# Kernel optimization log

Measured on AMD Instinct MI355X. Metric: run time of the kernel, lower is better.

Reference implementation:

```python
import jax, jax.numpy as jnp
import numpy as np


def bilinear_align_corners(p, H, W):
    # p: [B, C, h, w] -> [B, C, H, W], matches F.interpolate(mode='bilinear', align_corners=True)
    b, c, h, w = p.shape
    ys = jnp.linspace(0.0, h - 1.0, H)
    xs = jnp.linspace(0.0, w - 1.0, W)
    y0 = jnp.floor(ys).astype(jnp.int32)
    x0 = jnp.floor(xs).astype(jnp.int32)
    y1 = jnp.minimum(y0 + 1, h - 1)
    x1 = jnp.minimum(x0 + 1, w - 1)
    wy = (ys - y0.astype(p.dtype))[:, None]          # [H,1]
    wx = (xs - x0.astype(p.dtype))                   # [W]
    rows = p[:, :, y0, :] * (1 - wy) + p[:, :, y1, :] * wy   # [B,C,H,w]
    out = rows[:, :, :, x0] * (1 - wx) + rows[:, :, :, x1] * wx  # [B,C,H,W]
    return out


def conv1x1(x, W, b):
    return jnp.einsum('bchw,oc->bohw', x, W) + b[None, :, None, None]


def scan_axis(feat, A_bar, B_bar, axis):
    # selective recurrence h_i = A_i * stop_grad(h_{i-1}) + B_i * x_i along `axis`
    f = jnp.moveaxis(feat, axis, 0)
    A = jnp.moveaxis(A_bar, axis, 0)
    B = jnp.moveaxis(B_bar, axis, 0)

    def step(prev, inp):
        a_i, b_i, x_i = inp
        h = a_i * jax.lax.stop_gradient(prev) + b_i * x_i
        return h, h

    _, hs = jax.lax.scan(step, jnp.zeros_like(f[0]), (A, B, f))
    return jnp.moveaxis(hs, 0, axis)


def setup_inputs() -> dict:
    key = jax.random.key(0)
    ks = jax.random.split(key, 12)
    Bsz, Cin, H, W = 4, 64, 256, 256
    hid = 128
    s_in = 1.0 / np.sqrt(Cin)
    s_hid = 1.0 / np.sqrt(hid)
    return {
        'x': jax.random.normal(ks[0], (Bsz, Cin, H, W), jnp.float32),
        'prior': jax.random.normal(ks[1], (Bsz, 1, 64, 64), jnp.float32),
        'W_in': jax.random.uniform(ks[2], (hid, Cin), jnp.float32, -s_in, s_in),
        'b_in': jax.random.uniform(ks[3], (hid,), jnp.float32, -s_in, s_in),
        'W_out': jax.random.uniform(ks[4], (Cin, hid), jnp.float32, -s_hid, s_hid),
        'b_out': jax.random.uniform(ks[5], (Cin,), jnp.float32, -s_hid, s_hid),
        'W_delta': jax.random.uniform(ks[6], (hid, hid), jnp.float32, -s_hid, s_hid),
        'b_delta': jax.random.uniform(ks[7], (hid,), jnp.float32, -s_hid, s_hid),
        'W_B': jax.random.uniform(ks[8], (hid, hid), jnp.float32, -s_hid, s_hid),
        'b_B': jax.random.uniform(ks[9], (hid,), jnp.float32, -s_hid, s_hid),
        'A_param': jax.random.normal(ks[10], (hid,), jnp.float32),
        'lambda_delta': jnp.float32(0.1),
        'alpha': jnp.float32(0.1),
        'gamma': jnp.float32(0.1),
    }


def reference(x, prior, W_in, b_in, W_out, b_out, W_delta, b_delta, W_B, b_B,
              A_param, lambda_delta, alpha, gamma):
    Bsz, C, H, W = x.shape
    prior_up = jnp.clip(bilinear_align_corners(prior, H, W), -1.0, 1.0)
    x_proj = conv1x1(x, W_in, b_in)
    delta = jax.nn.softplus(conv1x1(x_proj, W_delta, b_delta) + lambda_delta * prior_up)
    B_k = conv1x1(x_proj, W_B, b_B) * (1.0 + alpha * prior_up)
    A = -jnp.exp(A_param)[None, :, None, None]
    A_bar = jnp.exp(delta * A)
    B_bar = delta * B_k
    # dim=0 in torch code scans along W (axis 3); dim=1 scans along H (axis 2)
    scanned = scan_axis(x_proj, A_bar, B_bar, 3) + scan_axis(x_proj, A_bar, B_bar, 2)
    out = conv1x1(scanned, W_out, b_out)
    return (x + gamma * out, prior_up)
```

## Files before the change

kernel.cpp:

```cpp
#include <hip/hip_runtime.h>
#include <hip/hip_bf16.h>

#define OUT1 16777216
#define BIG  33554432

typedef _Float16 half8 __attribute__((ext_vector_type(8)));
typedef float    floatx4 __attribute__((ext_vector_type(4)));

struct __align__(8) h4s { _Float16 x, y, z, w; };
__device__ inline void store4h(_Float16* p, float4 v){
    h4s t; t.x = (_Float16)v.x; t.y = (_Float16)v.y; t.z = (_Float16)v.z; t.w = (_Float16)v.w;
    *(h4s*)p = t;
}

__global__ __launch_bounds__(256) void k_prior(const float* __restrict__ prior, float* __restrict__ pu){
    int i = blockIdx.x*256 + threadIdx.x;
    int b = i >> 16;
    int rem = i & 65535;
    int yy = rem >> 8, xx = rem & 255;
    const float scale = 63.0f/255.0f;
    float sy = yy*scale, sx = xx*scale;
    int y0 = min((int)floorf(sy), 63), x0 = min((int)floorf(sx), 63);
    int y1 = min(y0+1, 63), x1 = min(x0+1, 63);
    float wy = sy - (float)y0, wx = sx - (float)x0;
    const float* pb = prior + (b<<12);
    float v00 = pb[(y0<<6)+x0], v01 = pb[(y0<<6)+x1];
    float v10 = pb[(y1<<6)+x0], v11 = pb[(y1<<6)+x1];
    float r0 = v00*(1.f-wy) + v10*wy;
    float r1 = v01*(1.f-wy) + v11*wy;
    float v  = r0*(1.f-wx) + r1*wx;
    pu[i] = fminf(fmaxf(v, -1.f), 1.f);
}

__global__ __launch_bounds__(256) void k_comb(const float* __restrict__ W_in, const float* __restrict__ b_in,
        const float* __restrict__ W_delta, const float* __restrict__ b_delta,
        const float* __restrict__ W_B, const float* __restrict__ b_B,
        const float* __restrict__ A_param, const float* __restrict__ W_out,
        _Float16* __restrict__ Wch, float* __restrict__ bcv, float* __restrict__ negA,
        _Float16* __restrict__ Wof, float* __restrict__ bct){
    int i = blockIdx.x*256 + threadIdx.x;
    if (i < 24576){
        int r = i >> 6, c = i & 63;
        float v;
        if (r < 128) v = W_in[i];
        else if (r < 256){
            int rr = r-128; float s = 0.f;
            for (int k=0;k<128;k++) s = fmaf(W_delta[(rr<<7)+k], W_in[(k<<6)+c], s);
            v = s;
        } else {
            int rr = r-256; float s = 0.f;
            for (int k=0;k<128;k++) s = fmaf(W_B[(rr<<7)+k], W_in[(k<<6)+c], s);
            v = s;
        }
        Wch[i] = (_Float16)v;
    } else if (i < 24960){
        int r = i - 24576; float v;
        if (r < 128) v = b_in[r];
        else if (r < 256){
            int rr=r-128; float s = b_delta[rr];
            for (int k=0;k<128;k++) s = fmaf(W_delta[(rr<<7)+k], b_in[k], s);
            v = s;
        } else {
            int rr=r-256; float s = b_B[rr];
            for (int k=0;k<128;k++) s = fmaf(W_B[(rr<<7)+k], b_in[k], s);
            v = s;
        }
        bcv[r] = v;
    } else if (i < 25088){
        negA[i-24960] = -expf(A_param[i-24960]);
    } else if (i < 33280){
        Wof[i-25088] = (_Float16)W_out[i-25088];
    } else if (i < 33792){
        int j = i - 33280;
        int c = j >> 2, comp = j & 3;
        float v;
        if (comp == 0) v = b_in[c];
        else if (comp == 1){
            float s = b_delta[c];
            for (int k=0;k<128;k++) s = fmaf(W_delta[(c<<7)+k], b_in[k], s);
            v = s;
        } else if (comp == 2){
            float s = b_B[c];
            for (int k=0;k<128;k++) s = fmaf(W_B[(c<<7)+k], b_in[k], s);
            v = s;
        } else {
            v = -expf(A_param[c]);
        }
        bct[j] = v;
    }
}

__global__ __launch_bounds__(512, 4) void k_proj_mfma(const float* __restrict__ x, const float* __restrict__ pu,
        const _Float16* __restrict__ Wch, const float* __restrict__ bct,
        const float* __restrict__ lam_p, const float* __restrict__ alp_p,
        _Float16* __restrict__ Ab, _Float16* __restrict__ Uu){
    __shared__ _Float16 Ws[24576];

    const int t    = threadIdx.x;
    const int lane = t & 63;
    const int wave = t >> 6;
    const int col  = lane & 15;
    const int quad = lane >> 4;

    const int bl      = blockIdx.x;
    const int b       = bl >> 7;
    const int px_base = (bl & 127) << 9;

    {
        const float4* wsrc = (const float4*)Wch;
        #pragma unroll
        for (int i = 0; i < 6; i++){
            int c = t + (i << 9);
            int row = c >> 3, part = c & 7;
            float4 v = wsrc[c];
            int byteoff = ((row << 7) + (part << 4)) ^ ((row & 7) << 4);
            *(float4*)((char*)Ws + byteoff) = v;
        }
    }

    const float lamv = lam_p[0], alpv = alp_p[0];
    const float* xcol = x + ((size_t)b<<22) + col;

    float xf0[8], xf1[8];
    {
        const float* xp = xcol + px_base + (wave<<4);
        #pragma unroll
        for (int j = 0; j < 8; j++){
            xf0[j] = xp[(size_t)(quad*8 + j) << 16];
            xf1[j] = xp[(size_t)(quad*8 + j + 32) << 16];
        }
    }

    __syncthreads();

    const int qb = quad << 4;
    const char* wsb = (const char*)Ws;

    #pragma unroll 1
    for (int ch = 0; ch < 4; ch++){
        const int pxw = px_base + (ch << 7) + (wave << 4);

        half8 aX0, aX1;
        #pragma unroll
        for (int j = 0; j < 8; j++){
            aX0[j] = (_Float16)xf0[j];
            aX1[j] = (_Float16)xf1[j];
        }

        if (ch < 3){
            const float* xn = xcol + pxw + 128;
            #pragma unroll
            for (int j = 0; j < 8; j++){
                xf0[j] = xn[(size_t)(quad*8 + j) << 16];
                xf1[j] = xn[(size_t)(quad*8 + j + 32) << 16];
            }
        }

        float4 puv4 = *(const float4*)(pu + (b<<16) + pxw + (quad<<2));
        float lpu[4], apu[4];
        #pragma unroll
        for (int r = 0; r < 4; r++){
            float pv = ((const float*)&puv4)[r];
            lpu[r] = lamv * pv;
            apu[r] = fmaf(alpv, pv, 1.f);
        }

        #pragma unroll 2
        for (int ct = 0; ct < 8; ct++){
            int rI = (ct << 4) + col;
            int xr = (rI & 7) << 4;
            half8 wI0 = *(const half8*)(wsb + ((( rI       << 7) +      qb) ^ xr));
            half8 wI1 = *(const half8*)(wsb + ((( rI       << 7) + 64 + qb) ^ xr));
            half8 wD0 = *(const half8*)(wsb + ((((rI + 128)<< 7) +      qb) ^ xr));
            half8 wD1 = *(const half8*)(wsb + ((((rI + 128)<< 7) + 64 + qb) ^ xr));
            half8 wB0 = *(const half8*)(wsb + ((((rI + 256)<< 7) +      qb) ^ xr));
            half8 wB1 = *(const half8*)(wsb + ((((rI + 256)<< 7) + 64 + qb) ^ xr));

            floatx4 aI = (floatx4){0.f,0.f,0.f,0.f};
            floatx4 aD = (floatx4){0.f,0.f,0.f,0.f};
            floatx4 aB = (floatx4){0.f,0.f,0.f,0.f};
            aI = __builtin_amdgcn_mfma_f32_16x16x32_f16(aX0, wI0, aI, 0, 0, 0);
            aD = __builtin_amdgcn_mfma_f32_16x16x32_f16(aX0, wD0, aD, 0, 0, 0);
            aB = __builtin_amdgcn_mfma_f32_16x16x32_f16(aX0, wB0, aB, 0, 0, 0);
            aI = __builtin_amdgcn_mfma_f32_16x16x32_f16(aX1, wI1, aI, 0, 0, 0);
            aD = __builtin_amdgcn_mfma_f32_16x16x32_f16(aX1, wD1, aD, 0, 0, 0);
            aB = __builtin_amdgcn_mfma_f32_16x16x32_f16(aX1, wB1, aB, 0, 0, 0);

            int c = (ct<<4) + col;
            float4 bv = *(const float4*)(bct + (c<<2));
            h4s oa, ou;
            #pragma unroll
            for (int r = 0; r < 4; r++){
                float sI = aI[r] + bv.x;
                float sD = aD[r] + bv.y;
                float sB = aB[r] + bv.z;
                float dpre  = sD + lpu[r];
                float delta = fmaxf(dpre, 0.f) + __logf(1.f + __expf(-fabsf(dpre)));
                float ab    = __expf(bv.w * delta);
                float uu    = delta * sB * apu[r] * sI;
                (&oa.x)[r] = (_Float16)ab;
                (&ou.x)[r] = (_Float16)uu;
            }
            size_t o = ((size_t)((b<<7) + c)<<16) + pxw + (quad<<2);
            *(h4s*)(Ab+o) = oa;
            *(h4s*)(Uu+o) = ou;
        }
    }
}

__global__ __launch_bounds__(256) void k_scan_w(const _Float16* __restrict__ Ab, const _Float16* __restrict__ Uu,
                                                _Float16* __restrict__ Sw){
    int r    = (blockIdx.x<<2) + (threadIdx.x>>6);
    int lane = threadIdx.x & 63;
    size_t base = ((size_t)r<<8) + (lane<<2);
    h4s a4 = *(const h4s*)(Ab+base);
    h4s u4 = *(const h4s*)(Uu+base);
    float ax=(float)a4.x, ay=(float)a4.y, az=(float)a4.z, aw=(float)a4.w;
    float ux=(float)u4.x, uy=(float)u4.y, uz=(float)u4.z, uw=(float)u4.w;
    float A = ax, U = ux;
    U = fmaf(ay, U, uy); A *= ay;
    U = fmaf(az, U, uz); A *= az;
    U = fmaf(aw, U, uw); A *= aw;
    #pragma unroll
    for (int off=1; off<64; off<<=1){
        float Apv = __shfl_up(A, off, 64);
        float Upv = __shfl_up(U, off, 64);
        if (lane >= off){ U = fmaf(A, Upv, U); A *= Apv; }
    }
    float h = __shfl_up(U, 1, 64);
    if (lane == 0) h = 0.f;
    float4 o;
    h = fmaf(ax, h, ux); o.x = h;
    h = fmaf(ay, h, uy); o.y = h;
    h = fmaf(az, h, uz); o.z = h;
    h = fmaf(aw, h, uw); o.w = h;
    store4h(Sw+base, o);
}

__global__ __launch_bounds__(256) void k_scan_h(const _Float16* __restrict__ AbH, const _Float16* __restrict__ UuH,
                                                const _Float16* __restrict__ Sw, _Float16* __restrict__ Sh){
    int t   = blockIdx.x*256 + threadIdx.x;
    int col = t >> 8;
    int w   = t & 255;
    size_t base = ((size_t)col<<16) + w;
    float h = 0.f;
    #pragma unroll 4
    for (int hh=0; hh<256; hh++){
        size_t idx = base + ((size_t)hh<<8);
        float a = (float)AbH[idx];
        float u = (float)UuH[idx];
        float s = (float)Sw[idx];
        h = fmaf(a, h, u);
        Sh[idx] = (_Float16)(h + s);
    }
}

__global__ __launch_bounds__(256, 4) void k_out_mfma(const float* __restrict__ x, const _Float16* __restrict__ Sh,
        const _Float16* __restrict__ Wof, const float* __restrict__ bout, const float* __restrict__ gam_p,
        float* __restrict__ out){
    const int t    = threadIdx.x;
    const int lane = t & 63;
    const int wave = t >> 6;
    const int col  = lane & 15;
    const int quad = lane >> 4;
    const int b    = blockIdx.x >> 8;
    const int p0   = (blockIdx.x & 255) << 8;
    const int wn0  = wave << 6;

    const _Float16* shb = Sh + ((size_t)b<<23) + p0 + wn0;

    floatx4 acc[4][4];
    #pragma unroll
    for (int mt = 0; mt < 4; mt++)
        #pragma unroll
        for (int nt = 0; nt < 4; nt++)
            acc[mt][nt] = (floatx4){0.f,0.f,0.f,0.f};

    #pragma unroll
    for (int kc = 0; kc < 4; kc++){
        half8 af[4];
        #pragma unroll
        for (int mt = 0; mt < 4; mt++)
            #pragma unroll
            for (int j = 0; j < 8; j++)
                af[mt][j] = shb[((size_t)(kc*32 + quad*8 + j)<<16) + mt*16 + col];
        half8 bf[4];
        #pragma unroll
        for (int nt = 0; nt < 4; nt++)
            bf[nt] = *(const half8*)(Wof + (nt*16 + col)*128 + kc*32 + quad*8);
        #pragma unroll
        for (int mt = 0; mt < 4; mt++)
            #pragma unroll
            for (int nt = 0; nt < 4; nt++)
                acc[mt][nt] = __builtin_amdgcn_mfma_f32_16x16x32_f16(af[mt], bf[nt], acc[mt][nt], 0, 0, 0);
    }

    const float gv = gam_p[0];
    #pragma unroll
    for (int nt = 0; nt < 4; nt++){
        int o = nt*16 + col;
        float bo = bout[o];
        #pragma unroll
        for (int mt = 0; mt < 4; mt++){
            size_t idx = (((size_t)(b*64 + o))<<16) + p0 + wn0 + mt*16 + (quad<<2);
            float4 xv = *(const float4*)(x + idx);
            float4 ov;
            ov.x = fmaf(gv, acc[mt][nt][0] + bo, xv.x);
            ov.y = fmaf(gv, acc[mt][nt][1] + bo, xv.y);
            ov.z = fmaf(gv, acc[mt][nt][2] + bo, xv.z);
            ov.w = fmaf(gv, acc[mt][nt][3] + bo, xv.w);
            *(float4*)(out + idx) = ov;
        }
    }
}

extern "C" void kernel_launch(void* const* d_in, const int* in_sizes, int n_in,
                              void* d_out, int out_size, void* d_ws, size_t ws_size,
                              hipStream_t stream){
    const float* x       = (const float*)d_in[0];
    const float* prior   = (const float*)d_in[1];
    const float* W_in    = (const float*)d_in[2];
    const float* b_in    = (const float*)d_in[3];
    const float* W_out   = (const float*)d_in[4];
    const float* b_out   = (const float*)d_in[5];
    const float* W_delta = (const float*)d_in[6];
    const float* b_delta = (const float*)d_in[7];
    const float* W_B     = (const float*)d_in[8];
    const float* b_B     = (const float*)d_in[9];
    const float* A_param = (const float*)d_in[10];
    const float* lam     = (const float*)d_in[11];
    const float* alp     = (const float*)d_in[12];
    const float* gam     = (const float*)d_in[13];

    float* out = (float*)d_out;
    float* pu  = out + OUT1;

    float* ws        = (float*)d_ws;
    _Float16* Wch    = (_Float16*)ws;
    float* bcv       = ws + 12288;
    float* negA      = ws + 12672;
    _Float16* Wof    = (_Float16*)(ws + 12800);
    float* bct       = ws + 16896;
    _Float16* AbH    = (_Float16*)(ws + 32768);
    _Float16* UuH    = AbH + BIG;
    _Float16* Sh     = UuH + BIG;
    _Float16* Sw     = (_Float16*)out;

    hipLaunchKernelGGL(k_prior,  dim3(1024),  dim3(256), 0, stream, prior, pu);
    hipLaunchKernelGGL(k_comb,   dim3(132),   dim3(256), 0, stream, W_in, b_in, W_delta, b_delta,
                       W_B, b_B, A_param, W_out, Wch, bcv, negA, Wof, bct);
    hipLaunchKernelGGL(k_proj_mfma, dim3(512), dim3(512), 0, stream,
                       x, pu, Wch, bct, lam, alp, AbH, UuH);
    hipLaunchKernelGGL(k_scan_w, dim3(32768), dim3(256), 0, stream, AbH, UuH, Sw);
    hipLaunchKernelGGL(k_scan_h, dim3(512),   dim3(256), 0, stream, AbH, UuH, Sw, Sh);
    hipLaunchKernelGGL(k_out_mfma, dim3(1024), dim3(256), 0, stream, x, Sh, Wof, b_out, gam, out);
}
```

Before: 331.2 us.

## Fuse W-direction and H-direction scans into one kernel per plane via shared memory

```diff
diff --git a/kernel.cpp b/kernel.cpp
--- a/kernel.cpp
+++ b/kernel.cpp
@@ -8,10 +8,6 @@
 typedef float    floatx4 __attribute__((ext_vector_type(4)));
 
 struct __align__(8) h4s { _Float16 x, y, z, w; };
-__device__ inline void store4h(_Float16* p, float4 v){
-    h4s t; t.x = (_Float16)v.x; t.y = (_Float16)v.y; t.z = (_Float16)v.z; t.w = (_Float16)v.w;
-    *(h4s*)p = t;
-}
 
 __global__ __launch_bounds__(256) void k_prior(const float* __restrict__ prior, float* __restrict__ pu){
     int i = blockIdx.x*256 + threadIdx.x;
@@ -208,50 +204,65 @@
     }
 }
 
-__global__ __launch_bounds__(256) void k_scan_w(const _Float16* __restrict__ Ab, const _Float16* __restrict__ Uu,
-                                                _Float16* __restrict__ Sw){
-    int r    = (blockIdx.x<<2) + (threadIdx.x>>6);
-    int lane = threadIdx.x & 63;
-    size_t base = ((size_t)r<<8) + (lane<<2);
-    h4s a4 = *(const h4s*)(Ab+base);
-    h4s u4 = *(const h4s*)(Uu+base);
-    float ax=(float)a4.x, ay=(float)a4.y, az=(float)a4.z, aw=(float)a4.w;
-    float ux=(float)u4.x, uy=(float)u4.y, uz=(float)u4.z, uw=(float)u4.w;
-    float A = ax, U = ux;
-    U = fmaf(ay, U, uy); A *= ay;
-    U = fmaf(az, U, uz); A *= az;
-    U = fmaf(aw, U, uw); A *= aw;
-    #pragma unroll
-    for (int off=1; off<64; off<<=1){
-        float Apv = __shfl_up(A, off, 64);
-        float Upv = __shfl_up(U, off, 64);
-        if (lane >= off){ U = fmaf(A, Upv, U); A *= Apv; }
-    }
-    float h = __shfl_up(U, 1, 64);
-    if (lane == 0) h = 0.f;
-    float4 o;
-    h = fmaf(ax, h, ux); o.x = h;
-    h = fmaf(ay, h, uy); o.y = h;
-    h = fmaf(az, h, uz); o.z = h;
-    h = fmaf(aw, h, uw); o.w = h;
-    store4h(Sw+base, o);
-}
-
-__global__ __launch_bounds__(256) void k_scan_h(const _Float16* __restrict__ AbH, const _Float16* __restrict__ UuH,
-                                                const _Float16* __restrict__ Sw, _Float16* __restrict__ Sh){
-    int t   = blockIdx.x*256 + threadIdx.x;
-    int col = t >> 8;
-    int w   = t & 255;
-    size_t base = ((size_t)col<<16) + w;
-    float h = 0.f;
-    #pragma unroll 4
-    for (int hh=0; hh<256; hh++){
-        size_t idx = base + ((size_t)hh<<8);
-        float a = (float)AbH[idx];
-        float u = (float)UuH[idx];
-        float s = (float)Sw[idx];
-        h = fmaf(a, h, u);
-        Sh[idx] = (_Float16)(h + s);
+__global__ __launch_bounds__(512) void k_scan_wh(const _Float16* __restrict__ Ab, const _Float16* __restrict__ Uu,
+                                                 _Float16* __restrict__ Sh){
+    __shared__ float As[8][256], Us[8][256], Wsc[8][256];
+
+    const int t    = threadIdx.x;
+    const int lane = t & 63;
+    const int wave = t >> 6;
+    const size_t plane = (size_t)blockIdx.x << 16;
+
+    float Hcol = 0.f;
+
+    size_t rb = plane + ((size_t)wave << 8) + (lane << 2);
+    h4s a4 = *(const h4s*)(Ab + rb);
+    h4s u4 = *(const h4s*)(Uu + rb);
+
+    #pragma unroll 1
+    for (int g = 0; g < 32; g++){
+        float ax=(float)a4.x, ay=(float)a4.y, az=(float)a4.z, aw=(float)a4.w;
+        float ux=(float)u4.x, uy=(float)u4.y, uz=(float)u4.z, uw=(float)u4.w;
+
+        if (g < 31){
+            size_t nb = plane + (((size_t)((g+1)<<3) + wave) << 8) + (lane << 2);
+            a4 = *(const h4s*)(Ab + nb);
+            u4 = *(const h4s*)(Uu + nb);
+        }
+
+        float A = ax, U = ux;
+        U = fmaf(ay, U, uy); A *= ay;
+        U = fmaf(az, U, uz); A *= az;
+        U = fmaf(aw, U, uw); A *= aw;
+        #pragma unroll
+        for (int off=1; off<64; off<<=1){
+            float Apv = __shfl_up(A, off, 64);
+            float Upv = __shfl_up(U, off, 64);
+            if (lane >= off){ U = fmaf(A, Upv, U); A *= Apv; }
+        }
+        float h = __shfl_up(U, 1, 64);
+        if (lane == 0) h = 0.f;
+        float4 o;
+        h = fmaf(ax, h, ux); o.x = h;
+        h = fmaf(ay, h, uy); o.y = h;
+        h = fmaf(az, h, uz); o.z = h;
+        h = fmaf(aw, h, uw); o.w = h;
+
+        int c0 = lane << 2;
+        *(float4*)&As [wave][c0] = (float4){ax,ay,az,aw};
+        *(float4*)&Us [wave][c0] = (float4){ux,uy,uz,uw};
+        *(float4*)&Wsc[wave][c0] = o;
+        __syncthreads();
+
+        if (t < 256){
+            size_t sb = plane + ((size_t)(g<<3) << 8) + t;
+            #pragma unroll
+            for (int v = 0; v < 8; v++){
+                Hcol = fmaf(As[v][t], Hcol, Us[v][t]);
+                Sh[sb + ((size_t)v<<8)] = (_Float16)(Hcol + Wsc[v][t]);
+            }
+        }
+        __syncthreads();
     }
 }
 
@@ -344,14 +355,12 @@
     _Float16* AbH    = (_Float16*)(ws + 32768);
     _Float16* UuH    = AbH + BIG;
     _Float16* Sh     = UuH + BIG;
-    _Float16* Sw     = (_Float16*)out;
 
     hipLaunchKernelGGL(k_prior,  dim3(1024),  dim3(256), 0, stream, prior, pu);
     hipLaunchKernelGGL(k_comb,   dim3(132),   dim3(256), 0, stream, W_in, b_in, W_delta, b_delta,
                        W_B, b_B, A_param, W_out, Wch, bcv, negA, Wof, bct);
     hipLaunchKernelGGL(k_proj_mfma, dim3(512), dim3(512), 0, stream,
                        x, pu, Wch, bct, lam, alp, AbH, UuH);
-    hipLaunchKernelGGL(k_scan_w, dim3(32768), dim3(256), 0, stream, AbH, UuH, Sw);
-    hipLaunchKernelGGL(k_scan_h, dim3(512),   dim3(256), 0, stream, AbH, UuH, Sw, Sh);
+    hipLaunchKernelGGL(k_scan_wh, dim3(512), dim3(512), 0, stream, AbH, UuH, Sh);
     hipLaunchKernelGGL(k_out_mfma, dim3(1024), dim3(256), 0, stream, x, Sh, Wof, b_out, gam, out);
 }
```

Result: faster. 284.1 us (-14.2%).
